# Optimization experiments

Measured on AMD Instinct MI355X. Metric: run time of the kernel, lower is better.

## Reference

```python
import jax, jax.numpy as jnp
import numpy as np

B, N, D, H, L, K, V = 2, 2048, 512, 8, 4, 32, 256
HD = D // H
MOD = 4294967296.0
SCALE = 1.0 / np.sqrt(HD)


def _ln(x, g, b):
    m = x.mean(-1, keepdims=True)
    v = ((x - m) ** 2).mean(-1, keepdims=True)
    return (x - m) * jax.lax.rsqrt(v + 1e-5) * g + b


def _expmap0(v, c):
    sc = jnp.sqrt(c)
    vn = jnp.maximum(jnp.linalg.norm(v, axis=-1, keepdims=True), 1e-8)
    return jnp.tanh(sc * vn) * v / (sc * vn)


def _knn_poincare(pos, c):
    xx = jnp.sum(pos ** 2, -1)                                    # [N]
    d2 = jnp.maximum(xx[:, None] + xx[None, :] - 2.0 * pos @ pos.T, 0.0)
    denom = (1.0 - c * xx)[:, None] * (1.0 - c * xx)[None, :] + 1e-8
    arg = jnp.maximum(1.0 + 2.0 * c * d2 / denom, 1.0)
    dist = jnp.arccosh(arg) / jnp.sqrt(c)                         # [N,N]
    neg_d, idx = jax.lax.top_k(-dist, K)                          # smallest-k
    return -neg_d, idx                                            # [N,K],[N,K]


def _forward(hashes, indices, emb, hash_proj, Wb, bb, log_c, pos_tangent,
             Wq, bq, Wk, bk, Wv, bv, Wo, bo, W1, b1, W2, b2,
             g1, be1, g2, be2, log_tau, Wout, bout):
    c = jnp.exp(log_c)
    char = emb[indices]                                           # [B,N,D]
    he = (hashes[..., None].astype(jnp.float32) / MOD) @ hash_proj  # [B,N,D]
    x = jnp.concatenate([char, he], -1) @ Wb + bb                 # [B,N,D]

    # kNN structure computed under no_grad in the original
    pos = _expmap0(jax.lax.stop_gradient(pos_tangent), jax.lax.stop_gradient(c))
    attn_dists, idx = _knn_poincare(pos, jax.lax.stop_gradient(c))  # shared over batch

    for i in range(L):
        xn = _ln(x, g1[i], be1[i])
        q = (xn @ Wq[i] + bq[i]).reshape(B, N, H, HD).transpose(0, 2, 1, 3)
        k = (xn @ Wk[i] + bk[i]).reshape(B, N, H, HD).transpose(0, 2, 1, 3)
        v = (xn @ Wv[i] + bv[i]).reshape(B, N, H, HD).transpose(0, 2, 1, 3)
        kg = k[:, :, idx, :]                                      # [B,H,N,K,HD]
        vg = v[:, :, idx, :]
        fs = jnp.einsum('bhnd,bhnkd->bhnk', q, kg) * SCALE
        gs = -attn_dists[None, None] / (jnp.exp(log_tau[i]) + 1e-8)
        p = jax.nn.softmax(fs + gs, axis=-1)                      # [B,H,N,K]
        ao = jnp.einsum('bhnk,bhnkd->bhnd', p, vg)
        ao = ao.transpose(0, 2, 1, 3).reshape(B, N, D)
        x = x + ao @ Wo[i] + bo[i]
        xn2 = _ln(x, g2[i], be2[i])
        x = x + jax.nn.gelu(xn2 @ W1[i] + b1[i], approximate=False) @ W2[i] + b2[i]

    return x[:, -1, :] @ Wout + bout                              # [B,V]


def setup_inputs():
    key = jax.random.key(0)
    ks = jax.random.split(key, 20)
    rn = lambda k, s, sc=0.02: jax.random.normal(k, s, jnp.float32) * sc
    z = lambda s: jnp.zeros(s, jnp.float32)
    o = lambda s: jnp.ones(s, jnp.float32)
    return {
        'hashes': jax.random.randint(ks[0], (B, N), 0, 1000000),
        'indices': jax.random.randint(ks[1], (B, N), 0, V),
        'emb': rn(ks[2], (V, D)),
        'hash_proj': rn(ks[3], (1, D)),
        'Wb': rn(ks[4], (2 * D, D)),
        'bb': z((D,)),
        'log_c': jnp.array(0.0, jnp.float32),
        'pos_tangent': rn(ks[5], (N, D)),
        'Wq': rn(ks[6], (L, D, D)), 'bq': z((L, D)),
        'Wk': rn(ks[7], (L, D, D)), 'bk': z((L, D)),
        'Wv': rn(ks[8], (L, D, D)), 'bv': z((L, D)),
        'Wo': rn(ks[9], (L, D, D)), 'bo': z((L, D)),
        'W1': rn(ks[10], (L, D, 4 * D)), 'b1': z((L, 4 * D)),
        'W2': rn(ks[11], (L, 4 * D, D)), 'b2': z((L, D)),
        'g1': o((L, D)), 'be1': z((L, D)),
        'g2': o((L, D)), 'be2': z((L, D)),
        'log_tau': z((L,)),
        'Wout': rn(ks[12], (D, V)), 'bout': z((V,)),
    }


def reference(hashes, indices, emb, hash_proj, Wb, bb, log_c, pos_tangent,
              Wq, bq, Wk, bk, Wv, bv, Wo, bo, W1, b1, W2, b2,
              g1, be1, g2, be2, log_tau, Wout, bout):
    return _forward(hashes, indices, emb, hash_proj, Wb, bb, log_c, pos_tangent,
                    Wq, bq, Wk, bk, Wv, bv, Wo, bo, W1, b1, W2, b2,
                    g1, be1, g2, be2, log_tau, Wout, bout)
```

## Files before the change

kernel.cpp:

```cpp
#include <hip/hip_runtime.h>
#include <hip/hip_bf16.h>
#include <math.h>

#define Bb 2
#define Nn 2048
#define Dd 512
#define Hh 8
#define Ll 4
#define Kk 32
#define Vv 256
#define HDh 64
#define Mrows (Bb*Nn)

static constexpr float SCALE_QK = 0.125f;
static constexpr float INV_MOD = 1.0f / 4294967296.0f;

typedef _Float16 f16;
typedef _Float16 f16x8 __attribute__((ext_vector_type(8)));
typedef _Float16 f16x4 __attribute__((ext_vector_type(4)));
typedef _Float16 f16x2 __attribute__((ext_vector_type(2)));
typedef float f32x4 __attribute__((ext_vector_type(4)));
typedef unsigned long long u64;

#define AS_GLOBAL(p) ((const __attribute__((address_space(1))) void*)(p))
#define AS_LDS(p)    ((__attribute__((address_space(3))) void*)(p))
__device__ __forceinline__ void gload16(const f16* g, f16* l) {
    __builtin_amdgcn_global_load_lds(AS_GLOBAL(g), AS_LDS(l), 16, 0, 0);
}

__global__ void scal_kernel(const float* __restrict__ log_c,
                            const float* __restrict__ log_tau,
                            float* __restrict__ scal) {
    int t = threadIdx.x;
    if (t == 0) {
        float c = expf(log_c[0]);
        scal[0] = c;
        scal[1] = sqrtf(c);
    }
    if (t < Ll) scal[2 + t] = 1.0f / (expf(log_tau[t]) + 1e-8f);
}

__global__ __launch_bounds__(256)
void hvec_part_kernel(const float* __restrict__ hash_proj,
                      const float* __restrict__ Wb,
                      float* __restrict__ part) {
    const int b = blockIdx.x;
    const int t = threadIdx.x;
    float a0 = 0.f, a1 = 0.f;
#pragma unroll
    for (int i = 0; i < 16; i++) {
        int kx = b * 16 + i;
        float hp = hash_proj[kx];
        const float* wr = Wb + (size_t)(Dd + kx) * Dd;
        a0 = fmaf(hp, wr[t], a0);
        a1 = fmaf(hp, wr[t + 256], a1);
    }
    part[b * Dd + t]       = a0;
    part[b * Dd + t + 256] = a1;
}
__global__ __launch_bounds__(256)
void hvec_red_kernel(const float* __restrict__ part, float* __restrict__ hvec) {
    const int n = blockIdx.x * 256 + threadIdx.x;
    float acc = 0.f;
#pragma unroll
    for (int b = 0; b < 32; b++) acc += part[b * Dd + n];
    hvec[n] = acc;
}

__global__ void conv_kernel(const float* __restrict__ src, f16* __restrict__ dst, int n) {
    int i = blockIdx.x * 256 + threadIdx.x;
    if (i < n) dst[i] = (f16)src[i];
}

__global__ void pack_bias_kernel(const float* __restrict__ bq, const float* __restrict__ bk,
                                 const float* __restrict__ bv, float* __restrict__ bqkv) {
    int t = blockIdx.x * 256 + threadIdx.x;
    int l = t / 1536, r = t % 1536;
    const float* src = (r < 512) ? bq : ((r < 1024) ? bk : bv);
    bqkv[t] = src[l * 512 + (r & 511)];
}

__global__ __launch_bounds__(256)
void trans_kernel(const float* __restrict__ src, f16* __restrict__ dst,
                  int K, int N, long sStride, long dStride) {
    __shared__ float tile[32][33];
    const float* s = src + blockIdx.z * sStride;
    f16* d = dst + blockIdx.z * dStride;
    int k0 = blockIdx.y * 32, n0 = blockIdx.x * 32;
    int tx = threadIdx.x & 31, ty = threadIdx.x >> 5;
#pragma unroll
    for (int i = 0; i < 32; i += 8)
        tile[ty + i][tx] = s[(long)(k0 + ty + i) * N + n0 + tx];
    __syncthreads();
#pragma unroll
    for (int i = 0; i < 32; i += 8)
        d[(long)(n0 + ty + i) * K + k0 + tx] = (f16)tile[tx][ty + i];
}

__global__ __launch_bounds__(256)
void trans4_kernel(const float* __restrict__ Wq, const float* __restrict__ Wk,
                   const float* __restrict__ Wv, const float* __restrict__ Wo,
                   f16* __restrict__ Wqkvt, f16* __restrict__ Wot) {
    __shared__ float tile[32][33];
    const int which = blockIdx.z >> 2, l = blockIdx.z & 3;
    const float* s;
    f16* d;
    switch (which) {
        case 0: s = Wq + (size_t)l * 262144; d = Wqkvt + (size_t)l * 786432;          break;
        case 1: s = Wk + (size_t)l * 262144; d = Wqkvt + (size_t)l * 786432 + 262144; break;
        case 2: s = Wv + (size_t)l * 262144; d = Wqkvt + (size_t)l * 786432 + 524288; break;
        default:s = Wo + (size_t)l * 262144; d = Wot   + (size_t)l * 262144;          break;
    }
    int k0 = blockIdx.y * 32, n0 = blockIdx.x * 32;
    int tx = threadIdx.x & 31, ty = threadIdx.x >> 5;
#pragma unroll
    for (int i = 0; i < 32; i += 8)
        tile[ty + i][tx] = s[(long)(k0 + ty + i) * 512 + n0 + tx];
    __syncthreads();
#pragma unroll
    for (int i = 0; i < 32; i += 8)
        d[(long)(n0 + ty + i) * 512 + k0 + tx] = (f16)tile[tx][ty + i];
}

template<int TN, bool GATHER, bool RANK1, bool GELU, bool RES, bool OUT16>
__global__ __launch_bounds__(256)
void mgemm(const f16* __restrict__ A, const f16* __restrict__ Wt,
           const float* __restrict__ bias,
           const int* __restrict__ gidx,
           const int* __restrict__ hashes, const float* __restrict__ hvec,
           const float* __restrict__ resid,
           void* __restrict__ Cout, int M, int N, int K) {
    constexpr int TM  = 64;
    constexpr int WRN = (TN == 64) ? 2 : 1;
    constexpr int WCN = 4 / WRN;
    constexpr int WRE = TM / WRN;
    constexpr int NIT = WRE / 16;
    constexpr int ACH = TM * 8;
    constexpr int BCH = TN * 8;
    constexpr int NCH = ACH + BCH;
    constexpr int NCHT = NCH / 256;
    __shared__ __align__(16) f16 sm[2][NCH * 8];
    const int t = threadIdx.x;
    const int lane = t & 63;
    const int w = t >> 6;
    const int wr = w / WCN, wc = w % WCN;
    const int i0 = blockIdx.y * TM, j0 = blockIdx.x * TN;

    const f16* gsrc[NCHT];
#pragma unroll
    for (int q = 0; q < NCHT; q++) {
        int c = t + q * 256;
        if (c < ACH) {
            int m = c >> 3, kb = (c & 7) ^ (m & 7);
            long row = GATHER ? (long)gidx[i0 + m] : (long)(i0 + m);
            gsrc[q] = A + row * K + kb * 8;
        } else {
            int cc = c - ACH;
            int n = cc >> 3, kb = (cc & 7) ^ (n & 7);
            gsrc[q] = Wt + (long)(j0 + n) * K + kb * 8;
        }
    }

    f32x4 acc[NIT][2];
#pragma unroll
    for (int i = 0; i < NIT; i++)
#pragma unroll
        for (int j = 0; j < 2; j++) acc[i][j] = (f32x4){0.f, 0.f, 0.f, 0.f};

#pragma unroll
    for (int q = 0; q < NCHT; q++)
        gload16(gsrc[q], &sm[0][(t + q * 256) * 8]);

    auto step = [&](int kt, const f16* rbuf, f16* wbuf) {
        asm volatile("s_waitcnt vmcnt(0)" ::: "memory");
        __syncthreads();
        if (kt + 64 < K) {
#pragma unroll
            for (int q = 0; q < NCHT; q++)
                gload16(gsrc[q] + kt + 64, wbuf + (t + q * 256) * 8);
        }
#pragma unroll
        for (int kh = 0; kh < 2; kh++) {
            f16x8 af[NIT], bf[2];
#pragma unroll
            for (int i = 0; i < NIT; i++) {
                int m = wr * WRE + i * 16 + (lane & 15);
                int sl = m * 8 + ((kh * 4 + (lane >> 4)) ^ (m & 7));
                af[i] = *(const f16x8*)(rbuf + sl * 8);
            }
#pragma unroll
            for (int j = 0; j < 2; j++) {
                int n = wc * 32 + j * 16 + (lane & 15);
                int sl = ACH + n * 8 + ((kh * 4 + (lane >> 4)) ^ (n & 7));
                bf[j] = *(const f16x8*)(rbuf + sl * 8);
            }
#pragma unroll
            for (int i = 0; i < NIT; i++)
#pragma unroll
                for (int j = 0; j < 2; j++)
                    acc[i][j] = __builtin_amdgcn_mfma_f32_16x16x32_f16(af[i], bf[j], acc[i][j], 0, 0, 0);
        }
    };

    for (int kt = 0; kt < K; kt += 128) {
        step(kt,      sm[0], sm[1]);
        step(kt + 64, sm[1], sm[0]);
    }

    float* Cf = (float*)Cout;
    f16*   Ch = (f16*)Cout;
#pragma unroll
    for (int i = 0; i < NIT; i++) {
        int rbase = i0 + wr * WRE + i * 16 + ((lane >> 4) << 2);
#pragma unroll
        for (int v = 0; v < 4; v++) {
            int row = rbase + v;
            float hterm = RANK1 ? (float)hashes[row] * INV_MOD : 0.f;
#pragma unroll
            for (int j = 0; j < 2; j++) {
                int col = j0 + wc * 32 + j * 16 + (lane & 15);
                float val = acc[i][j][v] + bias[col];
                if (RANK1) val += hterm * hvec[col];
                if (GELU)  val = 0.5f * val * (1.f + erff(val * 0.7071067811865475f));
                if (RES)   val += resid[(long)row * N + col];
                if (OUT16) Ch[(long)row * N + col] = (f16)val;
                else       Cf[(long)row * N + col] = val;
            }
        }
    }
}

__global__ __launch_bounds__(256)
void mdist_kernel(const f16* __restrict__ poshl, const float* __restrict__ xx,
                  const float* __restrict__ scal, float* __restrict__ dist) {
    constexpr int TM = 64, TN = 64;
    constexpr int ACH = TM * 8, BCH = TN * 8, NCH = ACH + BCH;
    constexpr int NCHT = NCH / 256;
    constexpr int KK = 1024;
    __shared__ __align__(16) f16 sm[2][NCH * 8];
    const int t = threadIdx.x;
    const int lane = t & 63;
    const int w = t >> 6;
    const int wr = w >> 1, wc = w & 1;
    const int i0 = blockIdx.y * TM, j0 = blockIdx.x * TN;

    const f16* gsrc[NCHT];
#pragma unroll
    for (int q = 0; q < NCHT; q++) {
        int c = t + q * 256;
        if (c < ACH) {
            int m = c >> 3, kb = (c & 7) ^ (m & 7);
            gsrc[q] = poshl + (long)(i0 + m) * KK + kb * 8;
        } else {
            int cc = c - ACH;
            int n = cc >> 3, kb = (cc & 7) ^ (n & 7);
            gsrc[q] = poshl + (long)(j0 + n) * KK + kb * 8;
        }
    }

    f32x4 acc[2][2];
#pragma unroll
    for (int i = 0; i < 2; i++)
#pragma unroll
        for (int j = 0; j < 2; j++) acc[i][j] = (f32x4){0.f, 0.f, 0.f, 0.f};

#pragma unroll
    for (int q = 0; q < NCHT; q++)
        gload16(gsrc[q], &sm[0][(t + q * 256) * 8]);

    auto step = [&](int kt, const f16* rbuf, f16* wbuf) {
        asm volatile("s_waitcnt vmcnt(0)" ::: "memory");
        __syncthreads();
        if (kt + 64 < KK) {
#pragma unroll
            for (int q = 0; q < NCHT; q++)
                gload16(gsrc[q] + kt + 64, wbuf + (t + q * 256) * 8);
        }
#pragma unroll
        for (int kh = 0; kh < 2; kh++) {
            f16x8 af[2], bf[2];
#pragma unroll
            for (int i = 0; i < 2; i++) {
                int m = wr * 32 + i * 16 + (lane & 15);
                int sl = m * 8 + ((kh * 4 + (lane >> 4)) ^ (m & 7));
                af[i] = *(const f16x8*)(rbuf + sl * 8);
            }
#pragma unroll
            for (int j = 0; j < 2; j++) {
                int n = wc * 32 + j * 16 + (lane & 15);
                int sl = ACH + n * 8 + ((kh * 4 + (lane >> 4)) ^ (n & 7));
                bf[j] = *(const f16x8*)(rbuf + sl * 8);
            }
#pragma unroll
            for (int i = 0; i < 2; i++)
#pragma unroll
                for (int j = 0; j < 2; j++)
                    acc[i][j] = __builtin_amdgcn_mfma_f32_16x16x32_f16(af[i], bf[j], acc[i][j], 0, 0, 0);
        }
    };

    for (int kt = 0; kt < KK; kt += 128) {
        step(kt,      sm[0], sm[1]);
        step(kt + 64, sm[1], sm[0]);
    }

    const float c = scal[0];
#pragma unroll
    for (int i = 0; i < 2; i++) {
        int rbase = i0 + wr * 32 + i * 16 + ((lane >> 4) << 2);
#pragma unroll
        for (int v = 0; v < 4; v++) {
            int row = rbase + v;
            float xi = xx[row];
#pragma unroll
            for (int j = 0; j < 2; j++) {
                int col = j0 + wc * 32 + j * 16 + (lane & 15);
                float xj = xx[col];
                float d2 = fmaxf(xi + xj - 2.f * acc[i][j][v], 0.f);
                float denom = (1.f - c * xi) * (1.f - c * xj) + 1e-8f;
                float arg = fmaxf(1.f + 2.f * c * d2 / denom, 1.f);
                dist[(long)row * Nn + col] = arg;
            }
        }
    }
}

__global__ __launch_bounds__(64)
void ln_kernel(const float* __restrict__ x, const float* __restrict__ g,
               const float* __restrict__ be, f16* __restrict__ xn) {
    const int row = blockIdx.x, t = threadIdx.x;
    const float4* xr = (const float4*)(x + (size_t)row * Dd);
    float4 v0 = xr[t], v1 = xr[t + 64];
    float s = v0.x + v0.y + v0.z + v0.w + v1.x + v1.y + v1.z + v1.w;
#pragma unroll
    for (int off = 32; off; off >>= 1) s += __shfl_xor(s, off, 64);
    float mean = s * (1.f / Dd);
    float d0x = v0.x - mean, d0y = v0.y - mean, d0z = v0.z - mean, d0w = v0.w - mean;
    float d1x = v1.x - mean, d1y = v1.y - mean, d1z = v1.z - mean, d1w = v1.w - mean;
    float q = d0x*d0x + d0y*d0y + d0z*d0z + d0w*d0w
            + d1x*d1x + d1y*d1y + d1z*d1z + d1w*d1w;
#pragma unroll
    for (int off = 32; off; off >>= 1) q += __shfl_xor(q, off, 64);
    float rstd = rsqrtf(q * (1.f / Dd) + 1e-5f);
    float4 g0 = ((const float4*)g)[t], g1v = ((const float4*)g)[t + 64];
    float4 b0 = ((const float4*)be)[t], b1v = ((const float4*)be)[t + 64];
    f16* xo = xn + (size_t)row * Dd;
    f16x4 o0, o1;
    o0[0] = (f16)(d0x * rstd * g0.x + b0.x);
    o0[1] = (f16)(d0y * rstd * g0.y + b0.y);
    o0[2] = (f16)(d0z * rstd * g0.z + b0.z);
    o0[3] = (f16)(d0w * rstd * g0.w + b0.w);
    o1[0] = (f16)(d1x * rstd * g1v.x + b1v.x);
    o1[1] = (f16)(d1y * rstd * g1v.y + b1v.y);
    o1[2] = (f16)(d1z * rstd * g1v.z + b1v.z);
    o1[3] = (f16)(d1w * rstd * g1v.w + b1v.w);
    *(f16x4*)(xo + t * 4)         = o0;
    *(f16x4*)(xo + (t + 64) * 4)  = o1;
}

__global__ __launch_bounds__(256)
void expmap_kernel(const float* __restrict__ vt, const float* __restrict__ scal,
                   f16* __restrict__ poshl, float* __restrict__ xx) {
    __shared__ float red[256];
    const int row = blockIdx.x, t = threadIdx.x;
    const float* vr = vt + (size_t)row * Dd;
    float v0 = vr[t], v1 = vr[t + 256];
    red[t] = v0 * v0 + v1 * v1;
    __syncthreads();
    for (int off = 128; off; off >>= 1) {
        if (t < off) red[t] += red[t + off];
        __syncthreads();
    }
    float total = red[0];
    float vn = fmaxf(sqrtf(total), 1e-8f);
    float sc = scal[1];
    float factor = tanhf(sc * vn) / (sc * vn);
    float p0 = factor * v0, p1 = factor * v1;
    f16 h0 = (f16)p0, h1 = (f16)p1;
    f16* pr = poshl + (size_t)row * 1024;
    pr[t]             = h0;
    pr[t + 256]       = h1;
    pr[512 + t]       = (f16)(p0 - (float)h0);
    pr[512 + t + 256] = (f16)(p1 - (float)h1);
    if (t == 0) xx[row] = factor * factor * total;
}

__global__ __launch_bounds__(256)
void topk_kernel(const float* __restrict__ dist, const float* __restrict__ scal,
                 float* __restrict__ outd, int* __restrict__ outi) {
    __shared__ unsigned wred[4];
    __shared__ unsigned bc;
    __shared__ __align__(8) u64 buf[128];
    const int t = threadIdx.x;
    const int w = t >> 6;
    const int n = blockIdx.x;
    const float sqc = scal[1];
    const uint4* dr = (const uint4*)(dist + (size_t)n * Nn);

    uint4 va = dr[t * 2];
    uint4 vb = dr[t * 2 + 1];
    unsigned k[8] = {va.x, va.y, va.z, va.w, vb.x, vb.y, vb.z, vb.w};
    const int g0 = t * 8;

    unsigned lo = 0x3F800000u;
    unsigned hi = 0x7F800001u;
    unsigned chi = 2048u;
    while (chi > 96u && (hi - lo) > 1u) {
        unsigned mid = lo + ((hi - lo) >> 1);
        int c = 0;
#pragma unroll
        for (int j = 0; j < 8; j++) c += (k[j] < mid) ? 1 : 0;
#pragma unroll
        for (int off = 32; off; off >>= 1) c += __shfl_xor(c, off, 64);
        __syncthreads();
        if ((t & 63) == 0) wred[w] = (unsigned)c;
        __syncthreads();
        unsigned ct = wred[0] + wred[1] + wred[2] + wred[3];
        if (ct >= 32u) { hi = mid; chi = ct; } else { lo = mid; }
    }

    if (chi <= 96u) {
        if (t == 0) bc = 0u;
        __syncthreads();
#pragma unroll
        for (int j = 0; j < 8; j++) {
            if (k[j] < hi) {
                unsigned s = atomicAdd(&bc, 1u);
                buf[s] = ((u64)k[j] << 11) | (u64)(unsigned)(g0 + j);
            }
        }
        __syncthreads();
        const int m = (int)chi;
        if (t < m) {
            u64 my = buf[t];
            int r = 0;
            for (int j = 0; j < m; j++) r += (buf[j] < my) ? 1 : 0;
            if (r < Kk) {
                float v = __uint_as_float((unsigned)(my >> 11));
                outd[n * Kk + r] = acoshf(v) / sqc;
                outi[n * Kk + r] = (int)(my & 2047u);
            }
        }
    } else {
        int c = 0;
#pragma unroll
        for (int j = 0; j < 8; j++) c += (k[j] < lo) ? 1 : 0;
#pragma unroll
        for (int off = 32; off; off >>= 1) c += __shfl_xor(c, off, 64);
        __syncthreads();
        if ((t & 63) == 0) wred[w] = (unsigned)c;
        if (t == 0) bc = 0u;
        __syncthreads();
        const int cless = (int)(wred[0] + wred[1] + wred[2] + wred[3]);
#pragma unroll
        for (int j = 0; j < 8; j++) {
            if (k[j] < lo) {
                unsigned s = atomicAdd(&bc, 1u);
                buf[s] = ((u64)k[j] << 11) | (u64)(unsigned)(g0 + j);
            }
        }
        __syncthreads();
        if (t < cless) {
            u64 my = buf[t];
            int r = 0;
            for (int j = 0; j < cless; j++) r += (buf[j] < my) ? 1 : 0;
            float v = __uint_as_float((unsigned)(my >> 11));
            outd[n * Kk + r] = acoshf(v) / sqc;
            outi[n * Kk + r] = (int)(my & 2047u);
        }
        const int need = Kk - cless;
        unsigned eqm = 0u;
#pragma unroll
        for (int j = 0; j < 8; j++) if (k[j] == lo) eqm |= (1u << j);
        const float dv = acoshf(__uint_as_float(lo)) / sqc;
        for (int s = 0; s < need; s++) {
            int mi = 0x7FFFFFFF;
#pragma unroll
            for (int j = 0; j < 8; j++)
                if (eqm & (1u << j)) mi = min(mi, g0 + j);
#pragma unroll
            for (int off = 32; off; off >>= 1) mi = min(mi, __shfl_xor(mi, off, 64));
            __syncthreads();
            if ((t & 63) == 0) wred[w] = (unsigned)mi;
            __syncthreads();
            int m4 = (int)min(min(wred[0], wred[1]), min(wred[2], wred[3]));
            int j = m4 - g0;
            if (j >= 0 && j < 8 && (eqm & (1u << j))) {
                eqm &= ~(1u << j);
                outd[n * Kk + cless + s] = dv;
                outi[n * Kk + cless + s] = m4;
            }
        }
    }
}

#define KVSTR 520
__global__ __launch_bounds__(256)
void attn_kernel(const f16* __restrict__ qkv, const float* __restrict__ adist,
                 const int* __restrict__ aidx, const float* __restrict__ scal,
                 int layer, f16* __restrict__ ao) {
    __shared__ __align__(16) f16 kv[64 * KVSTR];
    __shared__ __align__(16) f16 qs[512];
    __shared__ float ps[Hh][Kk];
    __shared__ float sdist[Kk];
    __shared__ int   sidx[Kk];
    const int t = threadIdx.x;
    const int b = blockIdx.x >> 11, n = blockIdx.x & (Nn - 1);
    const float inv_tau = scal[2 + layer];

    if (t < Kk) {
        sidx[t]  = aidx[n * Kk + t];
        sdist[t] = adist[n * Kk + t];
    }
    __syncthreads();

    {
        const size_t qrow = (size_t)(b * Nn + n) * 1536;
#pragma unroll
        for (int q = 0; q < 16; q++) {
            int c = q * 256 + t;
            int j = c >> 7, ci = c & 127;
            size_t src = (size_t)(b * Nn + sidx[j]) * 1536 + 512 + ci * 8;
            int dst = (ci < 64) ? (j * KVSTR + ci * 8)
                                : ((32 + j) * KVSTR + (ci - 64) * 8);
            *(f16x8*)(kv + dst) = *(const f16x8*)(qkv + src);
        }
        if (t < 64) *(f16x8*)(qs + t * 8) = *(const f16x8*)(qkv + qrow + t * 8);
    }
    __syncthreads();

    const int h = t >> 5, j = t & 31;
    float dot = 0.f;
#pragma unroll
    for (int i = 0; i < 8; i++) {
        f16x8 qa = *(const f16x8*)(qs + h * HDh + i * 8);
        f16x8 ka = *(const f16x8*)(kv + j * KVSTR + h * HDh + i * 8);
#pragma unroll
        for (int m = 0; m < 4; m++) {
            f16x2 qp = {qa[2 * m], qa[2 * m + 1]};
            f16x2 kp = {ka[2 * m], ka[2 * m + 1]};
            dot = __builtin_amdgcn_fdot2(qp, kp, dot, false);
        }
    }
    float s = dot * SCALE_QK - sdist[j] * inv_tau;
    float mx = s;
#pragma unroll
    for (int off = 16; off; off >>= 1) mx = fmaxf(mx, __shfl_xor(mx, off, 64));
    float e = expf(s - mx);
    float sum = e;
#pragma unroll
    for (int off = 16; off; off >>= 1) sum += __shfl_xor(sum, off, 64);
    ps[h][j] = e / sum;
    __syncthreads();

    const int d2 = t & 31;
    float a0 = 0.f, a1 = 0.f;
#pragma unroll
    for (int jj = 0; jj < Kk; jj++) {
        float p = ps[h][jj];
        f16x2 vv = *(const f16x2*)(kv + (32 + jj) * KVSTR + h * HDh + d2 * 2);
        a0 = fmaf(p, (float)vv[0], a0);
        a1 = fmaf(p, (float)vv[1], a1);
    }
    f16x2 outv; outv[0] = (f16)a0; outv[1] = (f16)a1;
    *(f16x2*)(ao + (size_t)(b * Nn + n) * Dd + h * HDh + d2 * 2) = outv;
}

__global__ void out_kernel(const float* __restrict__ x, const float* __restrict__ Wout,
                           const float* __restrict__ bout, float* __restrict__ out) {
    const int b = blockIdx.x, vc = threadIdx.x;
    const float* xr = x + ((size_t)(b * Nn + (Nn - 1))) * Dd;
    float acc = bout[vc];
    for (int d = 0; d < Dd; d++) acc = fmaf(xr[d], Wout[(size_t)d * Vv + vc], acc);
    out[b * Vv + vc] = acc;
}

static constexpr size_t X_OFF     = 0;
static constexpr size_t XN16_OFF  = 8388608;
static constexpr size_t QKV16_OFF = 12582912;
static constexpr size_t AO16_OFF  = 25165824;
static constexpr size_t H1_OFF    = 29360128;
static constexpr size_t AD_OFF    = 46137344;
static constexpr size_t AI_OFF    = 46399488;
static constexpr size_t SC_OFF    = 46661632;
static constexpr size_t HV_OFF    = 46661888;
static constexpr size_t XX_OFF    = 46663936;
static constexpr size_t BQKV_OFF  = 46672128;
static constexpr size_t EMB16_OFF = 46704896;
static constexpr size_t WBT_OFF   = 46967040;
static constexpr size_t WQKVT_OFF = 47491328;
static constexpr size_t WOT_OFF   = 53782784;
static constexpr size_t W1T_OFF   = 55879936;
static constexpr size_t W2T_OFF   = 64268544;
static constexpr size_t HP_OFF    = 72657152;

extern "C" void kernel_launch(void* const* d_in, const int* in_sizes, int n_in,
                              void* d_out, int out_size, void* d_ws, size_t ws_size,
                              hipStream_t stream) {
    (void)in_sizes; (void)n_in; (void)out_size; (void)ws_size;
    const int*   hashes    = (const int*)  d_in[0];
    const int*   indices   = (const int*)  d_in[1];
    const float* emb       = (const float*)d_in[2];
    const float* hash_proj = (const float*)d_in[3];
    const float* Wb        = (const float*)d_in[4];
    const float* bb        = (const float*)d_in[5];
    const float* log_c     = (const float*)d_in[6];
    const float* pos_t     = (const float*)d_in[7];
    const float* Wq        = (const float*)d_in[8];
    const float* bq        = (const float*)d_in[9];
    const float* Wk        = (const float*)d_in[10];
    const float* bk        = (const float*)d_in[11];
    const float* Wv        = (const float*)d_in[12];
    const float* bv        = (const float*)d_in[13];
    const float* Wo        = (const float*)d_in[14];
    const float* bo        = (const float*)d_in[15];
    const float* W1        = (const float*)d_in[16];
    const float* b1        = (const float*)d_in[17];
    const float* W2        = (const float*)d_in[18];
    const float* b2        = (const float*)d_in[19];
    const float* g1        = (const float*)d_in[20];
    const float* be1       = (const float*)d_in[21];
    const float* g2        = (const float*)d_in[22];
    const float* be2       = (const float*)d_in[23];
    const float* log_tau   = (const float*)d_in[24];
    const float* Wout      = (const float*)d_in[25];
    const float* bout      = (const float*)d_in[26];

    char* ws = (char*)d_ws;
    float* x      = (float*)(ws + X_OFF);
    f16*   xn16   = (f16*)  (ws + XN16_OFF);
    f16*   qkv16  = (f16*)  (ws + QKV16_OFF);
    f16*   ao16   = (f16*)  (ws + AO16_OFF);
    f16*   h1     = (f16*)  (ws + H1_OFF);
    float* adist  = (float*)(ws + AD_OFF);
    int*   aidx   = (int*)  (ws + AI_OFF);
    float* scal   = (float*)(ws + SC_OFF);
    float* hvec   = (float*)(ws + HV_OFF);
    float* xxb    = (float*)(ws + XX_OFF);
    float* bqkv   = (float*)(ws + BQKV_OFF);
    f16*   emb16  = (f16*)  (ws + EMB16_OFF);
    f16*   Wbt    = (f16*)  (ws + WBT_OFF);
    f16*   Wqkvt  = (f16*)  (ws + WQKVT_OFF);
    f16*   Wot    = (f16*)  (ws + WOT_OFF);
    f16*   W1t    = (f16*)  (ws + W1T_OFF);
    f16*   W2t    = (f16*)  (ws + W2T_OFF);
    float* hpart  = (float*)(ws + HP_OFF);
    f16*   poshl  = (f16*)  (ws + AO16_OFF);
    float* distb  = (float*)(ws + H1_OFF);

    scal_kernel<<<1, 64, 0, stream>>>(log_c, log_tau, scal);
    hvec_part_kernel<<<32, 256, 0, stream>>>(hash_proj, Wb, hpart);
    hvec_red_kernel<<<2, 256, 0, stream>>>(hpart, hvec);
    pack_bias_kernel<<<24, 256, 0, stream>>>(bq, bk, bv, bqkv);
    conv_kernel<<<(Vv * Dd + 255) / 256, 256, 0, stream>>>(emb, emb16, Vv * Dd);
    trans_kernel<<<dim3(16, 16, 1), 256, 0, stream>>>(Wb, Wbt, 512, 512, 0, 0);
    trans4_kernel<<<dim3(16, 16, 16), 256, 0, stream>>>(Wq, Wk, Wv, Wo, Wqkvt, Wot);
    trans_kernel<<<dim3(64, 16, Ll), 256, 0, stream>>>(W1, W1t, 512, 2048, 1048576, 1048576);
    trans_kernel<<<dim3(16, 64, Ll), 256, 0, stream>>>(W2, W2t, 2048, 512, 1048576, 1048576);

    mgemm<64, true, true, false, false, false><<<dim3(8, 64), 256, 0, stream>>>(
        emb16, Wbt, bb, indices, hashes, hvec, nullptr, x, Mrows, Dd, Dd);

    expmap_kernel<<<Nn, 256, 0, stream>>>(pos_t, scal, poshl, xxb);
    mdist_kernel<<<dim3(32, 32), 256, 0, stream>>>(poshl, xxb, scal, distb);
    topk_kernel<<<Nn, 256, 0, stream>>>(distb, scal, adist, aidx);

    for (int l = 0; l < Ll; l++) {
        ln_kernel<<<Mrows, 64, 0, stream>>>(x, g1 + l * Dd, be1 + l * Dd, xn16);
        mgemm<128, false, false, false, false, true><<<dim3(12, 64), 256, 0, stream>>>(
            xn16, Wqkvt + (size_t)l * 786432, bqkv + l * 1536,
            nullptr, nullptr, nullptr, nullptr, qkv16, Mrows, 1536, Dd);
        attn_kernel<<<Bb * Nn, 256, 0, stream>>>(qkv16, adist, aidx, scal, l, ao16);
        mgemm<64, false, false, false, true, false><<<dim3(8, 64), 256, 0, stream>>>(
            ao16, Wot + (size_t)l * 262144, bo + l * Dd,
            nullptr, nullptr, nullptr, x, x, Mrows, Dd, Dd);
        ln_kernel<<<Mrows, 64, 0, stream>>>(x, g2 + l * Dd, be2 + l * Dd, xn16);
        mgemm<128, false, false, true, false, true><<<dim3(16, 64), 256, 0, stream>>>(
            xn16, W1t + (size_t)l * 1048576, b1 + l * 4 * Dd,
            nullptr, nullptr, nullptr, nullptr, h1, Mrows, 4 * Dd, Dd);
        mgemm<64, false, false, false, true, false><<<dim3(8, 64), 256, 0, stream>>>(
            h1, W2t + (size_t)l * 1048576, b2 + l * Dd,
            nullptr, nullptr, nullptr, x, x, Mrows, Dd, 4 * Dd);
    }

    out_kernel<<<Bb, Vv, 0, stream>>>(x, Wout, bout, (float*)d_out);
}
```

Baseline: 627.8 us.

## Triple-buffer LDS pipeline in TN=64 GEMMs and distance kernel; batch LN rows

Switches the TN=64 mgemm variants and the Poincare distance GEMM from double to triple buffered LDS. Two tiles are kept in flight and the wait is partial (vmcnt(4)) rather than a full drain, so global loads overlap more with MFMA compute. Separately, layernorm now processes four rows per 256-thread block instead of one row per 64-thread block, which cuts the block count. Triple buffering uses more shared memory per block and may lower occupancy, and the vmcnt immediates assume exactly four loads per tile.

```diff
diff --git a/kernel.cpp b/kernel.cpp
--- a/kernel.cpp
+++ b/kernel.cpp
@@ -139,7 +139,8 @@
     constexpr int BCH = TN * 8;
     constexpr int NCH = ACH + BCH;
     constexpr int NCHT = NCH / 256;
-    __shared__ __align__(16) f16 sm[2][NCH * 8];
+    constexpr int NBUF = (TN == 64) ? 3 : 2;
+    __shared__ __align__(16) f16 sm[NBUF][NCH * 8];
     const int t = threadIdx.x;
     const int lane = t & 63;
     const int w = t >> 6;
@@ -167,18 +168,7 @@
 #pragma unroll
         for (int j = 0; j < 2; j++) acc[i][j] = (f32x4){0.f, 0.f, 0.f, 0.f};
 
-#pragma unroll
-    for (int q = 0; q < NCHT; q++)
-        gload16(gsrc[q], &sm[0][(t + q * 256) * 8]);
-
-    auto step = [&](int kt, const f16* rbuf, f16* wbuf) {
-        asm volatile("s_waitcnt vmcnt(0)" ::: "memory");
-        __syncthreads();
-        if (kt + 64 < K) {
-#pragma unroll
-            for (int q = 0; q < NCHT; q++)
-                gload16(gsrc[q] + kt + 64, wbuf + (t + q * 256) * 8);
-        }
+    auto compute = [&](const f16* rbuf) {
 #pragma unroll
         for (int kh = 0; kh < 2; kh++) {
             f16x8 af[NIT], bf[2];
@@ -202,9 +192,47 @@
         }
     };
 
-    for (int kt = 0; kt < K; kt += 128) {
-        step(kt,      sm[0], sm[1]);
-        step(kt + 64, sm[1], sm[0]);
+    if constexpr (TN == 64) {
+        static_assert(NCHT == 4, "vmcnt immediates assume NCHT==4");
+        const int T = K >> 6;
+#pragma unroll
+        for (int q = 0; q < NCHT; q++) gload16(gsrc[q],      &sm[0][(t + q * 256) * 8]);
+#pragma unroll
+        for (int q = 0; q < NCHT; q++) gload16(gsrc[q] + 64, &sm[1][(t + q * 256) * 8]);
+        f16 *bA = sm[0], *bB = sm[1], *bC = sm[2];
+        for (int tt = 0; tt < T - 1; ++tt) {
+            asm volatile("s_waitcnt vmcnt(4)" ::: "memory");
+            __syncthreads();
+            if (tt + 2 < T) {
+                const int kt2 = (tt + 2) << 6;
+#pragma unroll
+                for (int q = 0; q < NCHT; q++)
+                    gload16(gsrc[q] + kt2, bC + (t + q * 256) * 8);
+            }
+            compute(bA);
+            f16* tmp = bA; bA = bB; bB = bC; bC = tmp;
+        }
+        asm volatile("s_waitcnt vmcnt(0)" ::: "memory");
+        __syncthreads();
+        compute(bA);
+    } else {
+#pragma unroll
+        for (int q = 0; q < NCHT; q++)
+            gload16(gsrc[q], &sm[0][(t + q * 256) * 8]);
+        auto step = [&](int kt, const f16* rbuf, f16* wbuf) {
+            asm volatile("s_waitcnt vmcnt(0)" ::: "memory");
+            __syncthreads();
+            if (kt + 64 < K) {
+#pragma unroll
+                for (int q = 0; q < NCHT; q++)
+                    gload16(gsrc[q] + kt + 64, wbuf + (t + q * 256) * 8);
+            }
+            compute(rbuf);
+        };
+        for (int kt = 0; kt < K; kt += 128) {
+            step(kt,      sm[0], sm[1]);
+            step(kt + 64, sm[1], sm[0]);
+        }
     }
 
     float* Cf = (float*)Cout;
@@ -237,7 +265,7 @@
     constexpr int ACH = TM * 8, BCH = TN * 8, NCH = ACH + BCH;
     constexpr int NCHT = NCH / 256;
     constexpr int KK = 1024;
-    __shared__ __align__(16) f16 sm[2][NCH * 8];
+    __shared__ __align__(16) f16 sm[3][NCH * 8];
     const int t = threadIdx.x;
     const int lane = t & 63;
     const int w = t >> 6;
@@ -264,18 +292,7 @@
 #pragma unroll
         for (int j = 0; j < 2; j++) acc[i][j] = (f32x4){0.f, 0.f, 0.f, 0.f};
 
-#pragma unroll
-    for (int q = 0; q < NCHT; q++)
-        gload16(gsrc[q], &sm[0][(t + q * 256) * 8]);
-
-    auto step = [&](int kt, const f16* rbuf, f16* wbuf) {
-        asm volatile("s_waitcnt vmcnt(0)" ::: "memory");
-        __syncthreads();
-        if (kt + 64 < KK) {
-#pragma unroll
-            for (int q = 0; q < NCHT; q++)
-                gload16(gsrc[q] + kt + 64, wbuf + (t + q * 256) * 8);
-        }
+    auto compute = [&](const f16* rbuf) {
 #pragma unroll
         for (int kh = 0; kh < 2; kh++) {
             f16x8 af[2], bf[2];
@@ -299,10 +316,27 @@
         }
     };
 
-    for (int kt = 0; kt < KK; kt += 128) {
-        step(kt,      sm[0], sm[1]);
-        step(kt + 64, sm[1], sm[0]);
-    }
+#pragma unroll
+    for (int q = 0; q < NCHT; q++) gload16(gsrc[q],      &sm[0][(t + q * 256) * 8]);
+#pragma unroll
+    for (int q = 0; q < NCHT; q++) gload16(gsrc[q] + 64, &sm[1][(t + q * 256) * 8]);
+    f16 *bA = sm[0], *bB = sm[1], *bC = sm[2];
+    constexpr int T = KK >> 6;
+    for (int tt = 0; tt < T - 1; ++tt) {
+        asm volatile("s_waitcnt vmcnt(4)" ::: "memory");
+        __syncthreads();
+        if (tt + 2 < T) {
+            const int kt2 = (tt + 2) << 6;
+#pragma unroll
+            for (int q = 0; q < NCHT; q++)
+                gload16(gsrc[q] + kt2, bC + (t + q * 256) * 8);
+        }
+        compute(bA);
+        f16* tmp = bA; bA = bB; bB = bC; bC = tmp;
+    }
+    asm volatile("s_waitcnt vmcnt(0)" ::: "memory");
+    __syncthreads();
+    compute(bA);
 
     const float c = scal[0];
 #pragma unroll
@@ -325,10 +359,11 @@
     }
 }
 
-__global__ __launch_bounds__(64)
+__global__ __launch_bounds__(256)
 void ln_kernel(const float* __restrict__ x, const float* __restrict__ g,
                const float* __restrict__ be, f16* __restrict__ xn) {
-    const int row = blockIdx.x, t = threadIdx.x;
+    const int row = blockIdx.x * 4 + (threadIdx.x >> 6);
+    const int t = threadIdx.x & 63;
     const float4* xr = (const float4*)(x + (size_t)row * Dd);
     float4 v0 = xr[t], v1 = xr[t + 64];
     float s = v0.x + v0.y + v0.z + v0.w + v1.x + v1.y + v1.z + v1.w;
@@ -666,7 +701,7 @@
     topk_kernel<<<Nn, 256, 0, stream>>>(distb, scal, adist, aidx);
 
     for (int l = 0; l < Ll; l++) {
-        ln_kernel<<<Mrows, 64, 0, stream>>>(x, g1 + l * Dd, be1 + l * Dd, xn16);
+        ln_kernel<<<Mrows / 4, 256, 0, stream>>>(x, g1 + l * Dd, be1 + l * Dd, xn16);
         mgemm<128, false, false, false, false, true><<<dim3(12, 64), 256, 0, stream>>>(
             xn16, Wqkvt + (size_t)l * 786432, bqkv + l * 1536,
             nullptr, nullptr, nullptr, nullptr, qkv16, Mrows, 1536, Dd);
@@ -674,7 +709,7 @@
         mgemm<64, false, false, false, true, false><<<dim3(8, 64), 256, 0, stream>>>(
             ao16, Wot + (size_t)l * 262144, bo + l * Dd,
             nullptr, nullptr, nullptr, x, x, Mrows, Dd, Dd);
-        ln_kernel<<<Mrows, 64, 0, stream>>>(x, g2 + l * Dd, be2 + l * Dd, xn16);
+        ln_kernel<<<Mrows / 4, 256, 0, stream>>>(x, g2 + l * Dd, be2 + l * Dd, xn16);
         mgemm<128, false, false, true, false, true><<<dim3(16, 64), 256, 0, stream>>>(
             xn16, W1t + (size_t)l * 1048576, b1 + l * 4 * Dd,
             nullptr, nullptr, nullptr, nullptr, h1, Mrows, 4 * Dd, Dd);
```

Result: no change. 617.6 us (-1.6%).
